# Optimization experiments

Measured on AMD Instinct MI355X. Metric: run time of the kernel, lower is better.

## Reference

```python
import jax, jax.numpy as jnp
import numpy as np

B, S, D = 2, 2048, 1024
H, E = 16, 64


def setup_inputs() -> dict:
    key = jax.random.key(0)
    k1, k2, k3, k4 = jax.random.split(key, 4)
    x = jax.random.normal(k1, (B, S, D), dtype=jnp.float32)
    # per-head Q/K/V projection weights, stacked over the head axis
    scale = 1.0 / np.sqrt(D)
    Wq = jax.random.normal(k2, (H, D, E), dtype=jnp.float32) * scale
    Wk = jax.random.normal(k3, (H, D, E), dtype=jnp.float32) * scale
    Wv = jax.random.normal(k4, (H, D, E), dtype=jnp.float32) * scale
    return {"x": x, "Wq": Wq, "Wk": Wk, "Wv": Wv}


def reference(x, Wq, Wk, Wv):
    # Grouped-over-heads equivalent of the per-head torch loop.
    q = jnp.einsum("bsd,hde->bhse", x, Wq)  # [B,H,S,E]
    k = jnp.einsum("bsd,hde->bhse", x, Wk)
    v = jnp.einsum("bsd,hde->bhse", x, Wv)

    scores = jnp.einsum("bhse,bhte->bhst", q, k)  # [B,H,S,S]
    scores = scores / jnp.sqrt(jnp.asarray(E, dtype=scores.dtype))
    causal = jnp.tril(jnp.ones((S, S), dtype=bool))  # True on/below diagonal
    scores = jnp.where(causal, scores, jnp.finfo(scores.dtype).min)
    attn = jax.nn.softmax(scores, axis=-1)  # dropout p=0.0 -> identity

    out = jnp.einsum("bhst,bhte->bhse", attn, v)  # [B,H,S,E]
    # concat over heads on the last dim, matching torch.concat(..., dim=-1)
    return out.transpose(0, 2, 1, 3).reshape(B, S, H * E)
```

## Files before the change

### kernel.cpp

```cpp
#include <hip/hip_runtime.h>
#include <stdint.h>

#define S_LEN 2048
#define D_DIM 1024
#define NB 2
#define NH 16
#define NE 64
#define N_COLS (3 * NH * NE)
#define K_DIM D_DIM

typedef unsigned short u16;
typedef unsigned int u32;
typedef u16 u16x8 __attribute__((ext_vector_type(8)));
typedef __bf16 bf16x8 __attribute__((ext_vector_type(8)));
typedef __bf16 bf16x4 __attribute__((ext_vector_type(4)));
typedef float f32x4 __attribute__((ext_vector_type(4)));

__device__ __forceinline__ u16 f2b(float f) {
  u32 u = __builtin_bit_cast(u32, f);
  return (u16)((u + 0x7FFFu + ((u >> 16) & 1u)) >> 16);
}

__device__ __forceinline__ void gload_lds16(const void* g, void* l) {
  __builtin_amdgcn_global_load_lds(
      (const __attribute__((address_space(1))) u32*)g,
      (__attribute__((address_space(3))) u32*)l, 16, 0, 0);
}

__global__ __launch_bounds__(256) void k_prep(const float* __restrict__ x,
                                              const float* __restrict__ Wq,
                                              const float* __restrict__ Wk,
                                              const float* __restrict__ Wv,
                                              u16* __restrict__ xb,
                                              u16* __restrict__ Wt) {
  __shared__ u16 tile[64][65];
  int bid = blockIdx.x;
  int t = threadIdx.x;
  if (bid < 2048) {
    size_t i = (size_t)bid * 256 + t;
    const float4* xf = (const float4*)x;
    float4 a = xf[2 * i], c = xf[2 * i + 1];
    u16x8 o;
    o[0] = f2b(a.x); o[1] = f2b(a.y); o[2] = f2b(a.z); o[3] = f2b(a.w);
    o[4] = f2b(c.x); o[5] = f2b(c.y); o[6] = f2b(c.z); o[7] = f2b(c.w);
    *(u16x8*)(xb + 8 * i) = o;
  } else {
    int wbid = bid - 2048;
    int kb = wbid & 15;
    int h = (wbid >> 4) & 15;
    int proj = wbid >> 8;
    const float* W = (proj == 0) ? Wq : ((proj == 1) ? Wk : Wv);
    int k0 = kb * 64;
    int e = t & 63, kr = t >> 6;
    const float* src = W + ((size_t)h * D_DIM + k0 + kr * 16) * NE + e;
#pragma unroll
    for (int j = 0; j < 16; ++j) tile[kr * 16 + j][e] = f2b(src[(size_t)j * NE]);
    __syncthreads();
    int e2 = t >> 2, kc = (t & 3) * 16;
    u16x8 o0, o1;
#pragma unroll
    for (int j = 0; j < 8; ++j) { o0[j] = tile[kc + j][e2]; o1[j] = tile[kc + 8 + j][e2]; }
    size_t n = (size_t)proj * 1024 + h * 64 + e2;
    u16* dst = Wt + n * K_DIM + k0 + kc;
    *(u16x8*)dst = o0;
    *(u16x8*)(dst + 8) = o1;
  }
}

__global__ __launch_bounds__(256) void k_gemm(const u16* __restrict__ A,
                                              const u16* __restrict__ Bt,
                                              u16* __restrict__ C) {
  __shared__ __align__(16) u16 As[128 * 64];
  __shared__ __align__(16) u16 Bs[128 * 64];
  int t = threadIdx.x;
  int lane = t & 63, w = t >> 6;
  int wr = (w >> 1) * 64, wc = (w & 1) * 64;
  int bid = blockIdx.x;
  int xcd = bid & 7, r0 = bid >> 3;
  int m0 = (r0 / 3) * 128;
  int n0 = (xcd * 3 + (r0 % 3)) * 128;
  float qscale = ((n0 + wc) < 1024) ? 0.18033688f : 1.0f;
  f32x4 acc[4][4];
#pragma unroll
  for (int m = 0; m < 4; m++)
#pragma unroll
    for (int n = 0; n < 4; n++)
#pragma unroll
      for (int j = 0; j < 4; j++) acc[m][n][j] = 0.f;

  for (int k0 = 0; k0 < K_DIM; k0 += 64) {
#pragma unroll
    for (int i = 0; i < 4; ++i) {
      int ci = i * 256 + t;
      int row = ci >> 3, c = ci & 7;
      int cs = c ^ (row & 7);
      gload_lds16(A + (size_t)(m0 + row) * K_DIM + k0 + cs * 8,
                  (char*)As + (size_t)(i * 256 + w * 64) * 16);
      gload_lds16(Bt + (size_t)(n0 + row) * K_DIM + k0 + cs * 8,
                  (char*)Bs + (size_t)(i * 256 + w * 64) * 16);
    }
    __syncthreads();
#pragma unroll
    for (int ks = 0; ks < 2; ++ks) {
      int kc = ks * 4 + (lane >> 4);
      bf16x8 af[4], bfr[4];
#pragma unroll
      for (int m = 0; m < 4; m++) {
        int r = wr + m * 16 + (lane & 15);
        af[m] = *(const bf16x8*)&As[r * 64 + ((kc ^ (r & 7)) * 8)];
      }
#pragma unroll
      for (int n = 0; n < 4; n++) {
        int r = wc + n * 16 + (lane & 15);
        bfr[n] = *(const bf16x8*)&Bs[r * 64 + ((kc ^ (r & 7)) * 8)];
      }
#pragma unroll
      for (int m = 0; m < 4; m++)
#pragma unroll
        for (int n = 0; n < 4; n++)
          acc[m][n] = __builtin_amdgcn_mfma_f32_16x16x32_bf16(af[m], bfr[n], acc[m][n], 0, 0, 0);
    }
    __syncthreads();
  }
#pragma unroll
  for (int m = 0; m < 4; m++) {
#pragma unroll
    for (int r = 0; r < 4; r++) {
      int row = m0 + wr + m * 16 + (lane >> 4) * 4 + r;
#pragma unroll
      for (int n = 0; n < 4; n++) {
        int col = n0 + wc + n * 16 + (lane & 15);
        C[(size_t)row * N_COLS + col] = f2b(acc[m][n][r] * qscale);
      }
    }
  }
}

__device__ __forceinline__ void stage_k(const u16* kb_, u16* kdst, int kv0, int t, int w) {
#pragma unroll
  for (int i = 0; i < 2; ++i) {
    int ci = i * 256 + t;
    int row = ci >> 3, c = ci & 7;
    int cs = c ^ (row & 7);
    gload_lds16(kb_ + (size_t)(kv0 + row) * N_COLS + cs * 8,
                (char*)kdst + (size_t)(i * 256 + w * 64) * 16);
  }
}

__device__ __forceinline__ void vwrite(u16* vt, u16x8 va, u16x8 vb2, int vp, int vec) {
#pragma unroll
  for (int j = 0; j < 8; ++j) {
    int e = vec * 8 + j;
    int slot = (vp >> 2) ^ (e & 7) ^ (e >> 3);
    *(u32*)((char*)vt + e * 128 + slot * 16 + (vp & 3) * 4) =
        (u32)va[j] | ((u32)vb2[j] << 16);
  }
}

__global__ __launch_bounds__(256) void k_attn(const u16* __restrict__ qkv,
                                              float* __restrict__ out,
                                              float* __restrict__ O0,
                                              float* __restrict__ l0,
                                              float* __restrict__ l1) {
  __shared__ __align__(16) u16 Ks[2][64 * 64];
  __shared__ __align__(16) u16 Vt[2][64 * 64];
  int t = threadIdx.x;
  int lane = t & 63, w = t >> 6;
  int hi = lane >> 4, l15 = lane & 15;
  int bid = blockIdx.x;
  int x = bid & 7, r_ = bid >> 3;
  int bh = x * 4 + (r_ & 3);
  int u = r_ >> 2;
  int qt, c;
  if (u < 32) { qt = 31 - (u >> 1); c = u & 1; }
  else        { qt = 47 - u;        c = 0;     }
  int nt = qt + 1;
  int halfn = (nt + 1) >> 1;
  bool split = (u < 32);
  int lo = (split && c) ? halfn : 0;
  int te = split ? (c ? nt : halfn) : nt;
  int b = bh >> 4, h = bh & 15;
  const u16* qb_ = qkv + (size_t)b * S_LEN * N_COLS + h * NE;
  const u16* kb_ = qb_ + 1024;
  const u16* vb_ = qb_ + 2048;
  int vp = t >> 3, vec = t & 7;

  int q0 = qt * 64;
  int wqb = q0 + w * 16;

  bf16x8 qf[2];
#pragma unroll
  for (int ks = 0; ks < 2; ks++)
    qf[ks] = *(const bf16x8*)(qb_ + (size_t)(wqb + l15) * N_COLS + ks * 32 + hi * 8);

  f32x4 o[4];
#pragma unroll
  for (int i = 0; i < 4; i++)
#pragma unroll
    for (int j = 0; j < 4; j++) o[i][j] = 0.f;
  float lsum = 0.f;
  int myq = wqb + l15;

  stage_k(kb_, Ks[0], lo * 64, t, w);
  {
    const u16* vs = vb_ + (size_t)(lo * 64 + 2 * vp) * N_COLS + vec * 8;
    u16x8 va = *(const u16x8*)vs;
    u16x8 vb2 = *(const u16x8*)(vs + N_COLS);
    vwrite(Vt[0], va, vb2, vp, vec);
  }
  __syncthreads();

  int cur = 0;
  for (int ti = lo; ti < te; ++ti) {
    int kv0 = ti * 64;
    bool pf = (ti + 1 < te);
    u16x8 va, vb2;
    if (pf) {
      const u16* vs = vb_ + (size_t)(kv0 + 64 + 2 * vp) * N_COLS + vec * 8;
      va = *(const u16x8*)vs;
      vb2 = *(const u16x8*)(vs + N_COLS);
      stage_k(kb_, Ks[cur ^ 1], kv0 + 64, t, w);
    }

    f32x4 s[4];
#pragma unroll
    for (int f = 0; f < 4; f++)
#pragma unroll
      for (int j = 0; j < 4; j++) s[f][j] = 0.f;
    __builtin_amdgcn_s_setprio(1);
#pragma unroll
    for (int ks = 0; ks < 2; ks++) {
      int kc = ks * 4 + hi;
#pragma unroll
      for (int f = 0; f < 4; f++) {
        int r = f * 16 + l15;
        bf16x8 kf = *(const bf16x8*)&Ks[cur][r * 64 + ((kc ^ (r & 7)) * 8)];
        s[f] = __builtin_amdgcn_mfma_f32_16x16x32_bf16(kf, qf[ks], s[f], 0, 0, 0);
      }
    }
    __builtin_amdgcn_s_setprio(0);

    bool diag = (ti == nt - 1);
#pragma unroll
    for (int f = 0; f < 4; f++) {
#pragma unroll
      for (int r = 0; r < 4; r++) {
        float p = __builtin_amdgcn_exp2f(s[f][r]);
        if (diag) {
          int kv = kv0 + f * 16 + 4 * hi + r;
          p = (kv <= myq) ? p : 0.f;
        }
        s[f][r] = p;
        lsum += p;
      }
    }

    if (pf) vwrite(Vt[cur ^ 1], va, vb2, vp, vec);

    __builtin_amdgcn_s_setprio(1);
#pragma unroll
    for (int ks = 0; ks < 2; ks++) {
      bf16x8 pa;
#pragma unroll
      for (int j = 0; j < 4; j++) {
        pa[j] = (__bf16)s[2 * ks][j];
        pa[4 + j] = (__bf16)s[2 * ks + 1][j];
      }
      int kvo1 = 32 * ks + 4 * hi;
      int kvo2 = kvo1 + 16;
#pragma unroll
      for (int ef = 0; ef < 4; ef++) {
        int e = ef * 16 + l15;
        int sw = (e & 7) ^ (e >> 3);
        int a1 = e * 128 + (((kvo1 >> 3) ^ sw) * 16) + (kvo1 & 7) * 2;
        int a2 = e * 128 + (((kvo2 >> 3) ^ sw) * 16) + (kvo2 & 7) * 2;
        bf16x4 vlo = *(const bf16x4*)((const char*)Vt[cur] + a1);
        bf16x4 vhi = *(const bf16x4*)((const char*)Vt[cur] + a2);
        bf16x8 vbf;
#pragma unroll
        for (int j = 0; j < 4; j++) { vbf[j] = vlo[j]; vbf[4 + j] = vhi[j]; }
        o[ef] = __builtin_amdgcn_mfma_f32_16x16x32_bf16(pa, vbf, o[ef], 0, 0, 0);
      }
    }
    __builtin_amdgcn_s_setprio(0);
    __syncthreads();
    cur ^= 1;
  }

  lsum += __shfl_xor(lsum, 16);
  lsum += __shfl_xor(lsum, 32);

  if (!split) {
#pragma unroll
    for (int r = 0; r < 4; r++) {
      float l = __shfl(lsum, 4 * hi + r);
      float inv = 1.0f / l;
      int q = wqb + 4 * hi + r;
#pragma unroll
      for (int ef = 0; ef < 4; ef++) {
        int col = h * NE + ef * 16 + l15;
        out[((size_t)b * S_LEN + q) * (NH * NE) + col] = o[ef][r] * inv;
      }
    }
  } else {
    int sp = bh * 16 + (qt - 16);
    if (c == 0) {
#pragma unroll
      for (int r = 0; r < 4; r++) {
        int row = w * 16 + 4 * hi + r;
#pragma unroll
        for (int ef = 0; ef < 4; ef++)
          O0[(size_t)sp * 4096 + row * 64 + ef * 16 + l15] = o[ef][r];
      }
      if (lane < 16) l0[sp * 64 + w * 16 + l15] = lsum;
    } else {
#pragma unroll
      for (int r = 0; r < 4; r++) {
        int q = wqb + 4 * hi + r;
#pragma unroll
        for (int ef = 0; ef < 4; ef++) {
          int col = h * NE + ef * 16 + l15;
          out[((size_t)b * S_LEN + q) * (NH * NE) + col] = o[ef][r];
        }
      }
      if (lane < 16) l1[sp * 64 + w * 16 + l15] = lsum;
    }
  }
}

__global__ __launch_bounds__(256) void k_fix(float* __restrict__ out,
                                             const float* __restrict__ O0,
                                             const float* __restrict__ l0,
                                             const float* __restrict__ l1) {
  int f = (blockIdx.x * 256 + threadIdx.x) * 4;
  int sp = f >> 12;
  int row = (f >> 6) & 63;
  int e0 = f & 63;
  int bh = sp >> 4, qt = 16 + (sp & 15);
  int b = bh >> 4, h = bh & 15;
  int q = qt * 64 + row;
  float inv = 1.0f / (l0[sp * 64 + row] + l1[sp * 64 + row]);
  float4 p0 = *(const float4*)&O0[(size_t)sp * 4096 + row * 64 + e0];
  size_t oi = ((size_t)b * S_LEN + q) * (NH * NE) + h * NE + e0;
  float4 cu = *(float4*)&out[oi];
  float4 res;
  res.x = (cu.x + p0.x) * inv;
  res.y = (cu.y + p0.y) * inv;
  res.z = (cu.z + p0.z) * inv;
  res.w = (cu.w + p0.w) * inv;
  *(float4*)&out[oi] = res;
}

extern "C" void kernel_launch(void* const* d_in, const int* in_sizes, int n_in,
                              void* d_out, int out_size, void* d_ws, size_t ws_size,
                              hipStream_t stream) {
  const float* x = (const float*)d_in[0];
  const float* Wq = (const float*)d_in[1];
  const float* Wk = (const float*)d_in[2];
  const float* Wv = (const float*)d_in[3];
  float* out = (float*)d_out;

  char* ws = (char*)d_ws;
  u16* xb = (u16*)ws;
  u16* Wt = (u16*)(ws + (8u << 20));
  u16* qkv = (u16*)(ws + (14u << 20));
  float* O0 = (float*)ws;
  float* l0 = (float*)(ws + (8u << 20));
  float* l1 = (float*)(ws + (8u << 20) + (128u << 10));

  k_prep<<<dim3(2816), dim3(256), 0, stream>>>(x, Wq, Wk, Wv, xb, Wt);
  k_gemm<<<dim3(768), dim3(256), 0, stream>>>(xb, Wt, qkv);
  k_attn<<<dim3(1536), dim3(256), 0, stream>>>(qkv, out, O0, l0, l1);
  k_fix<<<dim3(2048), dim3(256), 0, stream>>>(out, O0, l0, l1);
}
```

Baseline: 100.2 us.

## Rebalance causal attention work by pairing long and short query tiles per block

Replaces the old split of long query tiles into halves plus standalone short tiles with a scheme where each block handles exactly 16-17 KV tiles. Type-A blocks process the first 17 KV tiles of a long query tile; type-B blocks finish the rest of a long tile and then a short tile, flushing the partial result in between. The grid drops from 1536 to 1024 blocks and the fix-up kernel is resized to match. The aim is equal per-block work and fewer blocks, at the cost of a mid-loop partial flush and heavier control flow in the kernel.

```diff
diff --git a/kernel.cpp b/kernel.cpp
--- a/kernel.cpp
+++ b/kernel.cpp
@@ -168,42 +168,47 @@
   int lane = t & 63, w = t >> 6;
   int hi = lane >> 4, l15 = lane & 15;
   int bid = blockIdx.x;
-  int x = bid & 7, r_ = bid >> 3;
-  int bh = x * 4 + (r_ & 3);
-  int u = r_ >> 2;
-  int qt, c;
-  if (u < 32) { qt = 31 - (u >> 1); c = u & 1; }
-  else        { qt = 47 - u;        c = 0;     }
-  int nt = qt + 1;
-  int halfn = (nt + 1) >> 1;
-  bool split = (u < 32);
-  int lo = (split && c) ? halfn : 0;
-  int te = split ? (c ? nt : halfn) : nt;
+  int x = bid & 7, g = bid >> 3;
+  int bh = x * 4 + (g & 3);
+  int u = g >> 2;
+  bool isA = (u < 16);
+  int p = isA ? u : u - 16;
+  int qt0 = 31 - p;
+  int qt1 = p;
+  int c0len = isA ? 17 : (15 - p);
+  int n_entries = isA ? 17 : 16;
+  int base0 = isA ? 0 : 17;
   int b = bh >> 4, h = bh & 15;
   const u16* qb_ = qkv + (size_t)b * S_LEN * N_COLS + h * NE;
   const u16* kb_ = qb_ + 1024;
   const u16* vb_ = qb_ + 2048;
   int vp = t >> 3, vec = t & 7;
 
-  int q0 = qt * 64;
-  int wqb = q0 + w * 16;
-
-  bf16x8 qf[2];
+  int wq0 = qt0 * 64 + w * 16;
+  int wq1 = qt1 * 64 + w * 16;
+  int myq0 = wq0 + l15, myq1 = wq1 + l15;
+
+  bf16x8 qf0[2], qf1[2];
 #pragma unroll
   for (int ks = 0; ks < 2; ks++)
-    qf[ks] = *(const bf16x8*)(qb_ + (size_t)(wqb + l15) * N_COLS + ks * 32 + hi * 8);
+    qf0[ks] = *(const bf16x8*)(qb_ + (size_t)(wq0 + l15) * N_COLS + ks * 32 + hi * 8);
+  if (!isA) {
+#pragma unroll
+    for (int ks = 0; ks < 2; ks++)
+      qf1[ks] = *(const bf16x8*)(qb_ + (size_t)(wq1 + l15) * N_COLS + ks * 32 + hi * 8);
+  }
 
   f32x4 o[4];
 #pragma unroll
   for (int i = 0; i < 4; i++)
 #pragma unroll
-    for (int j = 0; j < 4; j++) o[i][j] = 0.f;
+    for (int j2 = 0; j2 < 4; j2++) o[i][j2] = 0.f;
   float lsum = 0.f;
-  int myq = wqb + l15;
-
-  stage_k(kb_, Ks[0], lo * 64, t, w);
+
+  int ti0 = (c0len > 0) ? base0 : 0;
+  stage_k(kb_, Ks[0], ti0 * 64, t, w);
   {
-    const u16* vs = vb_ + (size_t)(lo * 64 + 2 * vp) * N_COLS + vec * 8;
+    const u16* vs = vb_ + (size_t)(ti0 * 64 + 2 * vp) * N_COLS + vec * 8;
     u16x8 va = *(const u16x8*)vs;
     u16x8 vb2 = *(const u16x8*)(vs + N_COLS);
     vwrite(Vt[0], va, vb2, vp, vec);
@@ -211,119 +216,141 @@
   __syncthreads();
 
   int cur = 0;
-  for (int ti = lo; ti < te; ++ti) {
-    int kv0 = ti * 64;
-    bool pf = (ti + 1 < te);
-    u16x8 va, vb2;
-    if (pf) {
-      const u16* vs = vb_ + (size_t)(kv0 + 64 + 2 * vp) * N_COLS + vec * 8;
-      va = *(const u16x8*)vs;
-      vb2 = *(const u16x8*)(vs + N_COLS);
-      stage_k(kb_, Ks[cur ^ 1], kv0 + 64, t, w);
-    }
-
-    f32x4 s[4];
-#pragma unroll
-    for (int f = 0; f < 4; f++)
-#pragma unroll
-      for (int j = 0; j < 4; j++) s[f][j] = 0.f;
-    __builtin_amdgcn_s_setprio(1);
-#pragma unroll
-    for (int ks = 0; ks < 2; ks++) {
-      int kc = ks * 4 + hi;
-#pragma unroll
-      for (int f = 0; f < 4; f++) {
-        int r = f * 16 + l15;
-        bf16x8 kf = *(const bf16x8*)&Ks[cur][r * 64 + ((kc ^ (r & 7)) * 8)];
-        s[f] = __builtin_amdgcn_mfma_f32_16x16x32_bf16(kf, qf[ks], s[f], 0, 0, 0);
-      }
-    }
-    __builtin_amdgcn_s_setprio(0);
-
-    bool diag = (ti == nt - 1);
-#pragma unroll
-    for (int f = 0; f < 4; f++) {
-#pragma unroll
-      for (int r = 0; r < 4; r++) {
-        float p = __builtin_amdgcn_exp2f(s[f][r]);
-        if (diag) {
-          int kv = kv0 + f * 16 + 4 * hi + r;
-          p = (kv <= myq) ? p : 0.f;
-        }
-        s[f][r] = p;
-        lsum += p;
-      }
-    }
-
-    if (pf) vwrite(Vt[cur ^ 1], va, vb2, vp, vec);
-
-    __builtin_amdgcn_s_setprio(1);
-#pragma unroll
-    for (int ks = 0; ks < 2; ks++) {
-      bf16x8 pa;
-#pragma unroll
-      for (int j = 0; j < 4; j++) {
-        pa[j] = (__bf16)s[2 * ks][j];
-        pa[4 + j] = (__bf16)s[2 * ks + 1][j];
-      }
-      int kvo1 = 32 * ks + 4 * hi;
-      int kvo2 = kvo1 + 16;
+
+#define ATTN_STEP(TI, QF, CQ, MYQ)                                              \
+  {                                                                             \
+    int kv0 = (TI) * 64;                                                        \
+    bool pf = (j + 1 < n_entries);                                              \
+    u16x8 va, vb2;                                                              \
+    if (pf) {                                                                   \
+      int tin = (j + 1 < c0len) ? (base0 + j + 1) : (j + 1 - c0len);            \
+      const u16* vs = vb_ + (size_t)(tin * 64 + 2 * vp) * N_COLS + vec * 8;     \
+      va = *(const u16x8*)vs;                                                   \
+      vb2 = *(const u16x8*)(vs + N_COLS);                                       \
+      stage_k(kb_, Ks[cur ^ 1], tin * 64, t, w);                                \
+    }                                                                           \
+    f32x4 s[4];                                                                 \
+    _Pragma("unroll") for (int f = 0; f < 4; f++)                               \
+        _Pragma("unroll") for (int j2 = 0; j2 < 4; j2++) s[f][j2] = 0.f;        \
+    __builtin_amdgcn_s_setprio(1);                                              \
+    _Pragma("unroll") for (int ks = 0; ks < 2; ks++) {                          \
+      int kc = ks * 4 + hi;                                                     \
+      _Pragma("unroll") for (int f = 0; f < 4; f++) {                           \
+        int r = f * 16 + l15;                                                   \
+        bf16x8 kf = *(const bf16x8*)&Ks[cur][r * 64 + ((kc ^ (r & 7)) * 8)];    \
+        s[f] = __builtin_amdgcn_mfma_f32_16x16x32_bf16(kf, QF[ks], s[f], 0, 0, 0); \
+      }                                                                         \
+    }                                                                           \
+    __builtin_amdgcn_s_setprio(0);                                              \
+    bool diag = ((TI) == (CQ));                                                 \
+    _Pragma("unroll") for (int f = 0; f < 4; f++) {                             \
+      float pr[4];                                                              \
+      _Pragma("unroll") for (int r = 0; r < 4; r++) {                           \
+        float pp = __builtin_amdgcn_exp2f(s[f][r]);                             \
+        if (diag) {                                                             \
+          int kv = kv0 + f * 16 + 4 * hi + r;                                   \
+          pp = (kv <= (MYQ)) ? pp : 0.f;                                        \
+        }                                                                       \
+        s[f][r] = pp;                                                           \
+        pr[r] = pp;                                                             \
+      }                                                                         \
+      lsum += (pr[0] + pr[1]) + (pr[2] + pr[3]);                                \
+    }                                                                           \
+    if (pf) vwrite(Vt[cur ^ 1], va, vb2, vp, vec);                              \
+    __builtin_amdgcn_s_setprio(1);                                              \
+    _Pragma("unroll") for (int ks = 0; ks < 2; ks++) {                          \
+      bf16x8 pa;                                                                \
+      _Pragma("unroll") for (int j2 = 0; j2 < 4; j2++) {                        \
+        pa[j2] = (__bf16)s[2 * ks][j2];                                         \
+        pa[4 + j2] = (__bf16)s[2 * ks + 1][j2];                                 \
+      }                                                                         \
+      int kvo1 = 32 * ks + 4 * hi;                                              \
+      int kvo2 = kvo1 + 16;                                                     \
+      _Pragma("unroll") for (int ef = 0; ef < 4; ef++) {                        \
+        int e = ef * 16 + l15;                                                  \
+        int sw = (e & 7) ^ (e >> 3);                                            \
+        int a1 = e * 128 + (((kvo1 >> 3) ^ sw) * 16) + (kvo1 & 7) * 2;          \
+        int a2 = e * 128 + (((kvo2 >> 3) ^ sw) * 16) + (kvo2 & 7) * 2;          \
+        bf16x4 vlo = *(const bf16x4*)((const char*)Vt[cur] + a1);               \
+        bf16x4 vhi2 = *(const bf16x4*)((const char*)Vt[cur] + a2);              \
+        bf16x8 vbf;                                                             \
+        _Pragma("unroll") for (int j2 = 0; j2 < 4; j2++) {                      \
+          vbf[j2] = vlo[j2];                                                    \
+          vbf[4 + j2] = vhi2[j2];                                               \
+        }                                                                       \
+        o[ef] = __builtin_amdgcn_mfma_f32_16x16x32_bf16(pa, vbf, o[ef], 0, 0, 0); \
+      }                                                                         \
+    }                                                                           \
+    __builtin_amdgcn_s_setprio(0);                                              \
+    __syncthreads();                                                            \
+    cur ^= 1;                                                                   \
+  }
+
+  int j = 0;
+  for (; j < c0len; ++j) ATTN_STEP(base0 + j, qf0, qt0, myq0);
+
+  if (!isA && c0len > 0) {
+    float ls = lsum;
+    ls += __shfl_xor(ls, 16);
+    ls += __shfl_xor(ls, 32);
+    int sp = bh * 15 + (qt0 - 17);
+#pragma unroll
+    for (int r = 0; r < 4; r++) {
+      int q = wq0 + 4 * hi + r;
 #pragma unroll
       for (int ef = 0; ef < 4; ef++) {
-        int e = ef * 16 + l15;
-        int sw = (e & 7) ^ (e >> 3);
-        int a1 = e * 128 + (((kvo1 >> 3) ^ sw) * 16) + (kvo1 & 7) * 2;
-        int a2 = e * 128 + (((kvo2 >> 3) ^ sw) * 16) + (kvo2 & 7) * 2;
-        bf16x4 vlo = *(const bf16x4*)((const char*)Vt[cur] + a1);
-        bf16x4 vhi = *(const bf16x4*)((const char*)Vt[cur] + a2);
-        bf16x8 vbf;
-#pragma unroll
-        for (int j = 0; j < 4; j++) { vbf[j] = vlo[j]; vbf[4 + j] = vhi[j]; }
-        o[ef] = __builtin_amdgcn_mfma_f32_16x16x32_bf16(pa, vbf, o[ef], 0, 0, 0);
-      }
-    }
-    __builtin_amdgcn_s_setprio(0);
-    __syncthreads();
-    cur ^= 1;
-  }
+        int col = h * NE + ef * 16 + l15;
+        out[((size_t)b * S_LEN + q) * (NH * NE) + col] = o[ef][r];
+      }
+    }
+    if (lane < 16) l1[sp * 64 + w * 16 + l15] = ls;
+#pragma unroll
+    for (int i = 0; i < 4; i++)
+#pragma unroll
+      for (int j2 = 0; j2 < 4; j2++) o[i][j2] = 0.f;
+    lsum = 0.f;
+  }
+
+  for (; j < n_entries; ++j) ATTN_STEP(j - c0len, qf1, qt1, myq1);
+#undef ATTN_STEP
 
   lsum += __shfl_xor(lsum, 16);
   lsum += __shfl_xor(lsum, 32);
-
-  if (!split) {
+  if (isA) {
+    if (p == 15) {
+#pragma unroll
+      for (int r = 0; r < 4; r++) {
+        float l = __shfl(lsum, 4 * hi + r);
+        float inv = 1.0f / l;
+        int q = wq0 + 4 * hi + r;
+#pragma unroll
+        for (int ef = 0; ef < 4; ef++) {
+          int col = h * NE + ef * 16 + l15;
+          out[((size_t)b * S_LEN + q) * (NH * NE) + col] = o[ef][r] * inv;
+        }
+      }
+    } else {
+      int sp = bh * 15 + (qt0 - 17);
+#pragma unroll
+      for (int r = 0; r < 4; r++) {
+        int row = w * 16 + 4 * hi + r;
+#pragma unroll
+        for (int ef = 0; ef < 4; ef++)
+          O0[(size_t)sp * 4096 + row * 64 + ef * 16 + l15] = o[ef][r];
+      }
+      if (lane < 16) l0[sp * 64 + w * 16 + l15] = lsum;
+    }
+  } else {
 #pragma unroll
     for (int r = 0; r < 4; r++) {
       float l = __shfl(lsum, 4 * hi + r);
       float inv = 1.0f / l;
-      int q = wqb + 4 * hi + r;
+      int q = wq1 + 4 * hi + r;
 #pragma unroll
       for (int ef = 0; ef < 4; ef++) {
         int col = h * NE + ef * 16 + l15;
         out[((size_t)b * S_LEN + q) * (NH * NE) + col] = o[ef][r] * inv;
       }
-    }
-  } else {
-    int sp = bh * 16 + (qt - 16);
-    if (c == 0) {
-#pragma unroll
-      for (int r = 0; r < 4; r++) {
-        int row = w * 16 + 4 * hi + r;
-#pragma unroll
-        for (int ef = 0; ef < 4; ef++)
-          O0[(size_t)sp * 4096 + row * 64 + ef * 16 + l15] = o[ef][r];
-      }
-      if (lane < 16) l0[sp * 64 + w * 16 + l15] = lsum;
-    } else {
-#pragma unroll
-      for (int r = 0; r < 4; r++) {
-        int q = wqb + 4 * hi + r;
-#pragma unroll
-        for (int ef = 0; ef < 4; ef++) {
-          int col = h * NE + ef * 16 + l15;
-          out[((size_t)b * S_LEN + q) * (NH * NE) + col] = o[ef][r];
-        }
-      }
-      if (lane < 16) l1[sp * 64 + w * 16 + l15] = lsum;
     }
   }
 }
@@ -336,7 +363,7 @@
   int sp = f >> 12;
   int row = (f >> 6) & 63;
   int e0 = f & 63;
-  int bh = sp >> 4, qt = 16 + (sp & 15);
+  int bh = sp / 15, qt = 17 + (sp % 15);
   int b = bh >> 4, h = bh & 15;
   int q = qt * 64 + row;
   float inv = 1.0f / (l0[sp * 64 + row] + l1[sp * 64 + row]);
@@ -366,10 +393,10 @@
   u16* qkv = (u16*)(ws + (14u << 20));
   float* O0 = (float*)ws;
   float* l0 = (float*)(ws + (8u << 20));
-  float* l1 = (float*)(ws + (8u << 20) + (128u << 10));
+  float* l1 = (float*)(ws + (8u << 20) + (256u << 10));
 
   k_prep<<<dim3(2816), dim3(256), 0, stream>>>(x, Wq, Wk, Wv, xb, Wt);
   k_gemm<<<dim3(768), dim3(256), 0, stream>>>(xb, Wt, qkv);
-  k_attn<<<dim3(1536), dim3(256), 0, stream>>>(qkv, out, O0, l0, l1);
-  k_fix<<<dim3(2048), dim3(256), 0, stream>>>(out, O0, l0, l1);
-}
+  k_attn<<<dim3(1024), dim3(256), 0, stream>>>(qkv, out, O0, l0, l1);
+  k_fix<<<dim3(1920), dim3(256), 0, stream>>>(out, O0, l0, l1);
+}
```

Result: slower. 103.0 us (+2.7%).
